# Kernel optimization log

Hardware: AMD Instinct MI355X
Metric: run time of the kernel (lower is better)

The kernel has to match this reference:

```python
import jax, jax.numpy as jnp
import numpy as np

N_NODES = 50000
N_EDGES = 800000
IN_CH = 256
H1, D1 = 4, 64   # layer 1: 4 heads x 64 -> 256
H2, D2 = 1, 64   # output layer: 1 head x 64
NEG_SLOPE = 0.2  # DGL GATConv default


def _leaky_relu(x):
    return jnp.where(x >= 0, x, NEG_SLOPE * x)


def gat_conv(h, src, dst, W, attn_l, attn_r, bias, res_W, num_heads, out_feats, apply_elu):
    """DGL GATConv (eval mode, feat_drop=attn_drop=0).
    h: (N, F_in); src/dst: (E,) edge endpoints (edge u->v aggregates at v).
    W: (F_in, H*D); attn_l/attn_r: (H, D); bias: (H*D,); res_W: (F_in, H*D) or None.
    Returns (N, H, D).
    """
    N = h.shape[0]
    ft = (h @ W).reshape(N, num_heads, out_feats)            # (N,H,D)
    el = jnp.sum(ft * attn_l, axis=-1)                        # (N,H)
    er = jnp.sum(ft * attn_r, axis=-1)                        # (N,H)
    e = _leaky_relu(el[src] + er[dst])                        # (E,H)
    # segment softmax over incoming edges of each dst node
    emax = jax.ops.segment_max(e, dst, num_segments=N)        # (N,H)
    emax = jax.lax.stop_gradient(emax)
    ee = jnp.exp(e - emax[dst])                               # (E,H)
    denom = jax.ops.segment_sum(ee, dst, num_segments=N)      # (N,H)
    a = ee / denom[dst]                                       # (E,H)
    msg = ft[src] * a[:, :, None]                             # (E,H,D)
    rst = jax.ops.segment_sum(msg, dst, num_segments=N)       # (N,H,D)
    if res_W is not None:
        rst = rst + (h @ res_W).reshape(N, num_heads, out_feats)
    rst = rst + bias.reshape(num_heads, out_feats)
    if apply_elu:
        rst = jax.nn.elu(rst)
    return rst


def setup_inputs() -> dict:
    key = jax.random.key(0)
    ks = jax.random.split(key, 12)
    feat = jax.random.normal(ks[0], (N_NODES, IN_CH), dtype=jnp.float32)
    src = jax.random.randint(ks[1], (N_EDGES,), 0, N_NODES)
    dst = jax.random.randint(ks[2], (N_EDGES,), 0, N_NODES)
    s = 0.1
    W1 = jax.random.normal(ks[3], (IN_CH, H1 * D1), dtype=jnp.float32) * s
    al1 = jax.random.normal(ks[4], (H1, D1), dtype=jnp.float32) * s
    ar1 = jax.random.normal(ks[5], (H1, D1), dtype=jnp.float32) * s
    b1 = jnp.zeros((H1 * D1,), dtype=jnp.float32)
    W2 = jax.random.normal(ks[6], (H1 * D1, H2 * D2), dtype=jnp.float32) * s
    al2 = jax.random.normal(ks[7], (H2, D2), dtype=jnp.float32) * s
    ar2 = jax.random.normal(ks[8], (H2, D2), dtype=jnp.float32) * s
    b2 = jnp.zeros((H2 * D2,), dtype=jnp.float32)
    resW2 = jax.random.normal(ks[9], (H1 * D1, H2 * D2), dtype=jnp.float32) * s
    return {"feat": feat, "src": src, "dst": dst,
            "W1": W1, "al1": al1, "ar1": ar1, "b1": b1,
            "W2": W2, "al2": al2, "ar2": ar2, "b2": b2, "resW2": resW2}


def reference(feat, src, dst, W1, al1, ar1, b1, W2, al2, ar2, b2, resW2):
    # Layer 1: 4 heads, ELU, no residual (first DGL layer built without residual)
    h = gat_conv(feat, src, dst, W1, al1, ar1, b1, None, H1, D1, True)
    h = h.reshape(N_NODES, H1 * D1)  # flatten(1)
    # Layer 2: 1 head, residual (linear res_fc since 256 != 64), no activation
    h = gat_conv(h, src, dst, W2, al2, ar2, b2, resW2, H2, D2, False)
    return h.mean(axis=1)  # mean over output heads -> (N, out_channels)
```

## Files before the change

kernel.cpp:

```cpp
#include <hip/hip_runtime.h>
#include <math.h>

#define N_NODES 50000
#define N_EDGES 800000
#define ELL_W 64

typedef __attribute__((ext_vector_type(8))) short bf16x8;
typedef __attribute__((ext_vector_type(4))) float f32x4;

__device__ __forceinline__ float leaky(float x) { return x >= 0.f ? x : 0.2f * x; }
__device__ __forceinline__ unsigned short f2bf(float f) {
  unsigned u = __float_as_uint(f);
  return (unsigned short)((u + 0x7fffu + ((u >> 16) & 1u)) >> 16);
}
__device__ __forceinline__ float bflo(unsigned u) { return __uint_as_float(u << 16); }
__device__ __forceinline__ float bfhi(unsigned u) { return __uint_as_float(u & 0xffff0000u); }
__device__ __forceinline__ unsigned pack2(float a, float b) {
  return (unsigned)f2bf(a) | ((unsigned)f2bf(b) << 16);
}

__launch_bounds__(256)
__global__ void prep_k(const float* __restrict__ feat, const float* __restrict__ W1,
                       const float* __restrict__ W2, const float* __restrict__ resW2,
                       short* __restrict__ featb, short* __restrict__ Wt1,
                       short* __restrict__ Wt2) {
  const int gtid = blockIdx.x * 256 + threadIdx.x;
  const int gsz = gridDim.x * 256;
  for (int idx = gtid; idx < 256 * 256; idx += gsz) {
    int n = idx >> 8, k = idx & 255;
    Wt1[idx] = (short)f2bf(W1[(size_t)k * 256 + n]);
  }
  for (int idx = gtid; idx < 128 * 256; idx += gsz) {
    int n = idx >> 8, k = idx & 255;
    float v = (n < 64) ? W2[(size_t)k * 64 + n] : resW2[(size_t)k * 64 + (n - 64)];
    Wt2[idx] = (short)f2bf(v);
  }
  const float4* f4 = (const float4*)feat;
  uint2* fb2 = (uint2*)featb;
  for (int idx = gtid; idx < N_NODES * 64; idx += gsz) {
    float4 f = f4[idx];
    uint2 o;
    o.x = pack2(f.x, f.y);
    o.y = pack2(f.z, f.w);
    fb2[idx] = o;
  }
}

template <int MODE, bool SCAT>
__launch_bounds__(256)
__global__ void mfma_gemm_k(const short* __restrict__ A, const short* __restrict__ Bt,
                            const float* __restrict__ bias, const float* __restrict__ al,
                            const float* __restrict__ ar, float* __restrict__ elp,
                            float* __restrict__ erp, short* __restrict__ Cb,
                            float* __restrict__ Cf, const int* __restrict__ src,
                            const int* __restrict__ dst, int* __restrict__ cnt,
                            int* __restrict__ ell, int M, int K, int N) {
  constexpr int EPI_COLS = (MODE == 0) ? 136 : 72;
  union SharedU {
    struct { short As[4][128][8]; short Bs[4][128][8]; } ab;
    short epi[128 * EPI_COLS];
  };
  __shared__ SharedU sh;

  if (SCAT && blockIdx.y == 2) {
    const int gtid = blockIdx.x * 256 + threadIdx.x;
    const int gsz = gridDim.x * 256;
    for (int e = gtid; e < N_EDGES; e += gsz) {
      int d = dst[e];
      int slot = atomicAdd(cnt + d, 1);
      if (slot < ELL_W) ell[d * ELL_W + slot] = src[e];
    }
    return;
  }
  const int tid = threadIdx.x;
  const int bm0 = blockIdx.x * 128, bn0 = blockIdx.y * 128;
  const int wave = tid >> 6, lane = tid & 63;
  const int wm = (wave & 1) * 64, wn = (wave >> 1) * 64;
  const int q = lane >> 4, r16 = lane & 15;
  const int srow = tid >> 1, sk = (tid & 1) * 16, sq = (tid & 1) * 2;
  f32x4 acc[4][4] = {};

  for (int k0 = 0; k0 < K; k0 += 32) {
    {
      uint4 v0 = {0, 0, 0, 0}, v1 = {0, 0, 0, 0};
      if (bm0 + srow < M) {
        const uint4* p = (const uint4*)(A + (size_t)(bm0 + srow) * K + k0 + sk);
        v0 = p[0];
        v1 = p[1];
      }
      *(uint4*)&sh.ab.As[sq][srow][0] = v0;
      *(uint4*)&sh.ab.As[sq + 1][srow][0] = v1;
    }
    {
      const uint4* p = (const uint4*)(Bt + (size_t)(bn0 + srow) * K + k0 + sk);
      *(uint4*)&sh.ab.Bs[sq][srow][0] = p[0];
      *(uint4*)&sh.ab.Bs[sq + 1][srow][0] = p[1];
    }
    __syncthreads();
    bf16x8 af[4], bfr[4];
#pragma unroll
    for (int i = 0; i < 4; ++i) af[i] = *(const bf16x8*)&sh.ab.As[q][wm + i * 16 + r16][0];
#pragma unroll
    for (int j = 0; j < 4; ++j) bfr[j] = *(const bf16x8*)&sh.ab.Bs[q][wn + j * 16 + r16][0];
#pragma unroll
    for (int i = 0; i < 4; ++i)
#pragma unroll
      for (int j = 0; j < 4; ++j)
        acc[i][j] = __builtin_amdgcn_mfma_f32_16x16x32_bf16(af[i], bfr[j], acc[i][j], 0, 0, 0);
    __syncthreads();
  }

  if (MODE == 0 || wn == 0) {
    const int head = (bn0 + wn) >> 6;
    float alv[4], arv[4];
#pragma unroll
    for (int j = 0; j < 4; ++j) {
      alv[j] = al[((MODE == 0) ? head * 64 : 0) + j * 16 + r16];
      arv[j] = ar[((MODE == 0) ? head * 64 : 0) + j * 16 + r16];
    }
#pragma unroll
    for (int i = 0; i < 4; ++i) {
#pragma unroll
      for (int reg = 0; reg < 4; ++reg) {
        float dl = acc[i][0][reg] * alv[0] + acc[i][1][reg] * alv[1] +
                   acc[i][2][reg] * alv[2] + acc[i][3][reg] * alv[3];
        float dr = acc[i][0][reg] * arv[0] + acc[i][1][reg] * arv[1] +
                   acc[i][2][reg] * arv[2] + acc[i][3][reg] * arv[3];
#pragma unroll
        for (int mm = 1; mm < 16; mm <<= 1) {
          dl += __shfl_xor(dl, mm);
          dr += __shfl_xor(dr, mm);
        }
        int row_g = bm0 + wm + i * 16 + q * 4 + reg;
        if (r16 == 0 && row_g < M) {
          if (MODE == 0) {
            elp[(size_t)row_g * 4 + head] = dl;
            erp[(size_t)row_g * 4 + head] = dr;
          } else {
            elp[row_g] = dl;
            erp[row_g] = dr;
          }
        }
      }
    }
  }

  if (MODE == 0) {
#pragma unroll
    for (int i = 0; i < 4; ++i)
#pragma unroll
      for (int reg = 0; reg < 4; ++reg) {
        int row = wm + i * 16 + q * 4 + reg;
#pragma unroll
        for (int j = 0; j < 4; ++j)
          sh.epi[row * EPI_COLS + wn + j * 16 + r16] = (short)f2bf(acc[i][j][reg]);
      }
    __syncthreads();
#pragma unroll
    for (int k = 0; k < 8; ++k) {
      int c = k * 256 + tid;
      int row = c >> 4, cc = c & 15;
      int row_g = bm0 + row;
      if (row_g < M) {
        uint4 v = *(const uint4*)&sh.epi[row * EPI_COLS + cc * 8];
        *(uint4*)(Cb + (size_t)row_g * N + bn0 + cc * 8) = v;
      }
    }
  } else {
    if (wn == 0) {
#pragma unroll
      for (int i = 0; i < 4; ++i)
#pragma unroll
        for (int reg = 0; reg < 4; ++reg) {
          int row = wm + i * 16 + q * 4 + reg;
#pragma unroll
          for (int j = 0; j < 4; ++j)
            sh.epi[row * EPI_COLS + j * 16 + r16] = (short)f2bf(acc[i][j][reg]);
        }
    } else {
#pragma unroll
      for (int i = 0; i < 4; ++i)
#pragma unroll
        for (int reg = 0; reg < 4; ++reg) {
          int row_g = bm0 + wm + i * 16 + q * 4 + reg;
          if (row_g >= M) continue;
#pragma unroll
          for (int j = 0; j < 4; ++j) {
            int col = j * 16 + r16;
            Cf[(size_t)row_g * 64 + col] = acc[i][j][reg] + bias[col];
          }
        }
    }
    __syncthreads();
#pragma unroll
    for (int k = 0; k < 4; ++k) {
      int c = k * 256 + tid;
      int row = c >> 3, cc = c & 7;
      int row_g = bm0 + row;
      if (row_g < M) {
        uint4 v = *(const uint4*)&sh.epi[row * EPI_COLS + cc * 8];
        *(uint4*)(Cb + (size_t)row_g * 64 + cc * 8) = v;
      }
    }
  }
}

__launch_bounds__(256)
__global__ void agg1_k(const int* __restrict__ ell, const int* __restrict__ cnt,
                       const float* __restrict__ el, const float* __restrict__ er,
                       const short* __restrict__ ft, const float* __restrict__ bias,
                       short* __restrict__ h1) {
  int node = blockIdx.x * 4 + (threadIdx.x >> 6);
  int lane = threadIdx.x & 63;
  if (node >= N_NODES) return;
  int deg = min(cnt[node], ELL_W);
  const int* row = ell + node * ELL_W;
  int h = lane >> 4;
  float erh = er[(size_t)node * 4 + h];
  float denom = 0.f;
  float4 acc = make_float4(0.f, 0.f, 0.f, 0.f);
  int i = 0;
  for (; i + 8 <= deg; i += 8) {
    int s[8];
#pragma unroll
    for (int k = 0; k < 8; ++k) s[k] = row[i + k];
    float e[8];
    uint2 u[8];
#pragma unroll
    for (int k = 0; k < 8; ++k) e[k] = leaky(el[(size_t)s[k] * 4 + h] + erh);
#pragma unroll
    for (int k = 0; k < 8; ++k) u[k] = *(const uint2*)(ft + (size_t)s[k] * 256 + lane * 4);
    float w[8];
#pragma unroll
    for (int k = 0; k < 8; ++k) w[k] = __expf(e[k]);
#pragma unroll
    for (int k = 0; k < 8; ++k) {
      denom += w[k];
      acc.x += w[k] * bflo(u[k].x);
      acc.y += w[k] * bfhi(u[k].x);
      acc.z += w[k] * bflo(u[k].y);
      acc.w += w[k] * bfhi(u[k].y);
    }
  }
  for (; i + 4 <= deg; i += 4) {
    int s0 = row[i + 0], s1 = row[i + 1], s2 = row[i + 2], s3 = row[i + 3];
    float e0 = leaky(el[(size_t)s0 * 4 + h] + erh);
    float e1 = leaky(el[(size_t)s1 * 4 + h] + erh);
    float e2 = leaky(el[(size_t)s2 * 4 + h] + erh);
    float e3 = leaky(el[(size_t)s3 * 4 + h] + erh);
    uint2 u0 = *(const uint2*)(ft + (size_t)s0 * 256 + lane * 4);
    uint2 u1 = *(const uint2*)(ft + (size_t)s1 * 256 + lane * 4);
    uint2 u2 = *(const uint2*)(ft + (size_t)s2 * 256 + lane * 4);
    uint2 u3 = *(const uint2*)(ft + (size_t)s3 * 256 + lane * 4);
    float w0 = __expf(e0), w1 = __expf(e1), w2 = __expf(e2), w3 = __expf(e3);
    denom += (w0 + w1) + (w2 + w3);
    acc.x += (w0 * bflo(u0.x) + w1 * bflo(u1.x)) + (w2 * bflo(u2.x) + w3 * bflo(u3.x));
    acc.y += (w0 * bfhi(u0.x) + w1 * bfhi(u1.x)) + (w2 * bfhi(u2.x) + w3 * bfhi(u3.x));
    acc.z += (w0 * bflo(u0.y) + w1 * bflo(u1.y)) + (w2 * bflo(u2.y) + w3 * bflo(u3.y));
    acc.w += (w0 * bfhi(u0.y) + w1 * bfhi(u1.y)) + (w2 * bfhi(u2.y) + w3 * bfhi(u3.y));
  }
  for (; i < deg; ++i) {
    int s = row[i];
    float e = leaky(el[(size_t)s * 4 + h] + erh);
    uint2 u = *(const uint2*)(ft + (size_t)s * 256 + lane * 4);
    float w = __expf(e);
    denom += w;
    acc.x += w * bflo(u.x);
    acc.y += w * bfhi(u.x);
    acc.z += w * bflo(u.y);
    acc.w += w * bfhi(u.y);
  }
  float inv = (deg > 0) ? 1.f / denom : 0.f;
  float4 b = *(const float4*)(bias + lane * 4);
  float4 v;
  v.x = acc.x * inv + b.x;
  v.y = acc.y * inv + b.y;
  v.z = acc.z * inv + b.z;
  v.w = acc.w * inv + b.w;
  v.x = v.x > 0.f ? v.x : expm1f(v.x);
  v.y = v.y > 0.f ? v.y : expm1f(v.y);
  v.z = v.z > 0.f ? v.z : expm1f(v.z);
  v.w = v.w > 0.f ? v.w : expm1f(v.w);
  uint2 o;
  o.x = pack2(v.x, v.y);
  o.y = pack2(v.z, v.w);
  *(uint2*)(h1 + (size_t)node * 256 + lane * 4) = o;
}

__launch_bounds__(256)
__global__ void agg2_k(const int* __restrict__ ell, const int* __restrict__ cnt,
                       const float* __restrict__ el, const float* __restrict__ er,
                       const short* __restrict__ ft, float* __restrict__ out) {
  int node = blockIdx.x * 4 + (threadIdx.x >> 6);
  int lane = threadIdx.x & 63;
  if (node >= N_NODES) return;
  int deg = min(cnt[node], ELL_W);
  const int* row = ell + node * ELL_W;
  float erd = er[node];
  float denom = 0.f, acc = 0.f;
  int i = 0;
  for (; i + 8 <= deg; i += 8) {
    int s[8];
#pragma unroll
    for (int k = 0; k < 8; ++k) s[k] = row[i + k];
    float e[8], f[8];
#pragma unroll
    for (int k = 0; k < 8; ++k) e[k] = leaky(el[s[k]] + erd);
#pragma unroll
    for (int k = 0; k < 8; ++k)
      f[k] = bflo((unsigned)(unsigned short)ft[(size_t)s[k] * 64 + lane]);
#pragma unroll
    for (int k = 0; k < 8; ++k) {
      float w = __expf(e[k]);
      denom += w;
      acc += w * f[k];
    }
  }
  for (; i < deg; ++i) {
    int s = row[i];
    float e = leaky(el[s] + erd);
    float f = bflo((unsigned)(unsigned short)ft[(size_t)s * 64 + lane]);
    float w = __expf(e);
    denom += w;
    acc += w * f;
  }
  float r = (deg > 0) ? acc / denom : 0.f;
  out[(size_t)node * 64 + lane] += r;
}

extern "C" void kernel_launch(void* const* d_in, const int* in_sizes, int n_in,
                              void* d_out, int out_size, void* d_ws, size_t ws_size,
                              hipStream_t stream) {
  const float* feat  = (const float*)d_in[0];
  const int*   src   = (const int*)d_in[1];
  const int*   dst   = (const int*)d_in[2];
  const float* W1    = (const float*)d_in[3];
  const float* al1   = (const float*)d_in[4];
  const float* ar1   = (const float*)d_in[5];
  const float* b1    = (const float*)d_in[6];
  const float* W2    = (const float*)d_in[7];
  const float* al2   = (const float*)d_in[8];
  const float* ar2   = (const float*)d_in[9];
  const float* b2    = (const float*)d_in[10];
  const float* resW2 = (const float*)d_in[11];
  float* out = (float*)d_out;

  char* p = (char*)d_ws;
  short* featb = (short*)p; p += (size_t)N_NODES * 256 * 2;
  short* ft1b = (short*)p; p += (size_t)N_NODES * 256 * 2;
  short* h1b  = (short*)p; p += (size_t)N_NODES * 256 * 2;
  short* ft2b = (short*)p; p += (size_t)N_NODES * 64 * 2;
  short* Wt1  = (short*)p; p += 256 * 256 * 2;
  short* Wt2  = (short*)p; p += 128 * 256 * 2;
  float* el1  = (float*)p; p += (size_t)N_NODES * 4 * 4;
  float* er1  = (float*)p; p += (size_t)N_NODES * 4 * 4;
  float* el2  = (float*)p; p += (size_t)N_NODES * 4;
  float* er2  = (float*)p; p += (size_t)N_NODES * 4;
  int* cnt    = (int*)p;   p += (size_t)N_NODES * 4;
  int* ell    = (int*)p;   p += (size_t)N_NODES * ELL_W * 4;

  hipMemsetAsync(cnt, 0, (size_t)N_NODES * sizeof(int), stream);

  dim3 blk(256);

  prep_k<<<2048, blk, 0, stream>>>(feat, W1, W2, resW2, featb, Wt1, Wt2);

  mfma_gemm_k<0, true><<<dim3(391, 3), blk, 0, stream>>>(
      featb, Wt1, nullptr, al1, ar1, el1, er1, ft1b, nullptr,
      src, dst, cnt, ell, N_NODES, 256, 256);
  agg1_k<<<12500, blk, 0, stream>>>(ell, cnt, el1, er1, ft1b, b1, h1b);

  mfma_gemm_k<1, false><<<dim3(391, 1), blk, 0, stream>>>(
      h1b, Wt2, b2, al2, ar2, el2, er2, ft2b, out,
      nullptr, nullptr, nullptr, nullptr, N_NODES, 256, 128);
  agg2_k<<<12500, blk, 0, stream>>>(ell, cnt, el2, er2, ft2b, out);
}
```

Before: 289.9 us.

## Fuse feature bf16 conversion into GEMM load and move edge slot atomics to prep

Removes the separate fp32-to-bf16 pass over the node features: the layer-1 GEMM now loads fp32 feat directly and packs it to bf16 while staging into shared memory. The per-edge atomic slot assignment moves into the prep kernel, which records an 8-bit slot per edge, so the scatter blocks in the GEMM only write ELL entries. The epilogue LDS row padding also changes. This saves a full write and re-read of the bf16 feature copy, but the GEMM reads twice as many bytes per A tile and gains an extra byte array per edge.

```diff
diff --git a/kernel.cpp b/kernel.cpp
--- a/kernel.cpp
+++ b/kernel.cpp
@@ -20,10 +20,10 @@
 }
 
 __launch_bounds__(256)
-__global__ void prep_k(const float* __restrict__ feat, const float* __restrict__ W1,
-                       const float* __restrict__ W2, const float* __restrict__ resW2,
-                       short* __restrict__ featb, short* __restrict__ Wt1,
-                       short* __restrict__ Wt2) {
+__global__ void prep_k(const float* __restrict__ W1, const float* __restrict__ W2,
+                       const float* __restrict__ resW2, const int* __restrict__ dst,
+                       short* __restrict__ Wt1, short* __restrict__ Wt2,
+                       int* __restrict__ cnt, unsigned char* __restrict__ slot8) {
   const int gtid = blockIdx.x * 256 + threadIdx.x;
   const int gsz = gridDim.x * 256;
   for (int idx = gtid; idx < 256 * 256; idx += gsz) {
@@ -35,27 +35,23 @@
     float v = (n < 64) ? W2[(size_t)k * 64 + n] : resW2[(size_t)k * 64 + (n - 64)];
     Wt2[idx] = (short)f2bf(v);
   }
-  const float4* f4 = (const float4*)feat;
-  uint2* fb2 = (uint2*)featb;
-  for (int idx = gtid; idx < N_NODES * 64; idx += gsz) {
-    float4 f = f4[idx];
-    uint2 o;
-    o.x = pack2(f.x, f.y);
-    o.y = pack2(f.z, f.w);
-    fb2[idx] = o;
+  for (int e = gtid; e < N_EDGES; e += gsz) {
+    int s = atomicAdd(cnt + dst[e], 1);
+    slot8[e] = (unsigned char)min(s, 255);
   }
 }
 
 template <int MODE, bool SCAT>
 __launch_bounds__(256)
-__global__ void mfma_gemm_k(const short* __restrict__ A, const short* __restrict__ Bt,
+__global__ void mfma_gemm_k(const void* __restrict__ Ap, const short* __restrict__ Bt,
                             const float* __restrict__ bias, const float* __restrict__ al,
                             const float* __restrict__ ar, float* __restrict__ elp,
                             float* __restrict__ erp, short* __restrict__ Cb,
                             float* __restrict__ Cf, const int* __restrict__ src,
-                            const int* __restrict__ dst, int* __restrict__ cnt,
+                            const int* __restrict__ dst,
+                            const unsigned char* __restrict__ slot8,
                             int* __restrict__ ell, int M, int K, int N) {
-  constexpr int EPI_COLS = (MODE == 0) ? 136 : 72;
+  constexpr int EPI_COLS = (MODE == 0) ? 140 : 76;
   union SharedU {
     struct { short As[4][128][8]; short Bs[4][128][8]; } ab;
     short epi[128 * EPI_COLS];
@@ -66,9 +62,8 @@
     const int gtid = blockIdx.x * 256 + threadIdx.x;
     const int gsz = gridDim.x * 256;
     for (int e = gtid; e < N_EDGES; e += gsz) {
-      int d = dst[e];
-      int slot = atomicAdd(cnt + d, 1);
-      if (slot < ELL_W) ell[d * ELL_W + slot] = src[e];
+      int slot = slot8[e];
+      if (slot < ELL_W) ell[(size_t)dst[e] * ELL_W + slot] = src[e];
     }
     return;
   }
@@ -81,7 +76,25 @@
   f32x4 acc[4][4] = {};
 
   for (int k0 = 0; k0 < K; k0 += 32) {
-    {
+    if (MODE == 0) {
+      const float* A = (const float*)Ap;
+      float4 f0 = {0, 0, 0, 0}, f1 = f0, f2 = f0, f3 = f0;
+      if (bm0 + srow < M) {
+        const float4* p = (const float4*)(A + (size_t)(bm0 + srow) * K + k0 + sk);
+        f0 = p[0];
+        f1 = p[1];
+        f2 = p[2];
+        f3 = p[3];
+      }
+      uint4 v0, v1;
+      v0.x = pack2(f0.x, f0.y); v0.y = pack2(f0.z, f0.w);
+      v0.z = pack2(f1.x, f1.y); v0.w = pack2(f1.z, f1.w);
+      v1.x = pack2(f2.x, f2.y); v1.y = pack2(f2.z, f2.w);
+      v1.z = pack2(f3.x, f3.y); v1.w = pack2(f3.z, f3.w);
+      *(uint4*)&sh.ab.As[sq][srow][0] = v0;
+      *(uint4*)&sh.ab.As[sq + 1][srow][0] = v1;
+    } else {
+      const short* A = (const short*)Ap;
       uint4 v0 = {0, 0, 0, 0}, v1 = {0, 0, 0, 0};
       if (bm0 + srow < M) {
         const uint4* p = (const uint4*)(A + (size_t)(bm0 + srow) * K + k0 + sk);
@@ -214,7 +227,7 @@
   int lane = threadIdx.x & 63;
   if (node >= N_NODES) return;
   int deg = min(cnt[node], ELL_W);
-  const int* row = ell + node * ELL_W;
+  const int* row = ell + (size_t)node * ELL_W;
   int h = lane >> 4;
   float erh = er[(size_t)node * 4 + h];
   float denom = 0.f;
@@ -295,7 +308,7 @@
   int lane = threadIdx.x & 63;
   if (node >= N_NODES) return;
   int deg = min(cnt[node], ELL_W);
-  const int* row = ell + node * ELL_W;
+  const int* row = ell + (size_t)node * ELL_W;
   float erd = er[node];
   float denom = 0.f, acc = 0.f;
   int i = 0;
@@ -346,7 +359,6 @@
   float* out = (float*)d_out;
 
   char* p = (char*)d_ws;
-  short* featb = (short*)p; p += (size_t)N_NODES * 256 * 2;
   short* ft1b = (short*)p; p += (size_t)N_NODES * 256 * 2;
   short* h1b  = (short*)p; p += (size_t)N_NODES * 256 * 2;
   short* ft2b = (short*)p; p += (size_t)N_NODES * 64 * 2;
@@ -357,17 +369,18 @@
   float* el2  = (float*)p; p += (size_t)N_NODES * 4;
   float* er2  = (float*)p; p += (size_t)N_NODES * 4;
   int* cnt    = (int*)p;   p += (size_t)N_NODES * 4;
-  int* ell    = (int*)p;   p += (size_t)N_NODES * ELL_W * 4;
+  unsigned char* slot8 = (unsigned char*)p; p += (size_t)N_EDGES;
+  int* ell    = (int*)p;
 
   hipMemsetAsync(cnt, 0, (size_t)N_NODES * sizeof(int), stream);
 
   dim3 blk(256);
 
-  prep_k<<<2048, blk, 0, stream>>>(feat, W1, W2, resW2, featb, Wt1, Wt2);
+  prep_k<<<2048, blk, 0, stream>>>(W1, W2, resW2, dst, Wt1, Wt2, cnt, slot8);
 
   mfma_gemm_k<0, true><<<dim3(391, 3), blk, 0, stream>>>(
-      featb, Wt1, nullptr, al1, ar1, el1, er1, ft1b, nullptr,
-      src, dst, cnt, ell, N_NODES, 256, 256);
+      feat, Wt1, nullptr, al1, ar1, el1, er1, ft1b, nullptr,
+      src, dst, slot8, ell, N_NODES, 256, 256);
   agg1_k<<<12500, blk, 0, stream>>>(ell, cnt, el1, er1, ft1b, b1, h1b);
 
   mfma_gemm_k<1, false><<<dim3(391, 1), blk, 0, stream>>>(
```

Measured after the change: 293.6 us. No clear change (+1.3%).
